# Kernel tuning notes

Measured on AMD Instinct MI355X. Metric: run time of the kernel, lower is better.

## Reference

```python
import jax, jax.numpy as jnp
import numpy as np

# ---- static config (matches init_kwargs) ----
N_BANDS = 8
WIN = 2048
R = 0.5
SR = 16000
STRIDE = WIN - int(R * WIN)  # 1024
Q = 0.707  # torchaudio default Q for high/lowpass_biquad


def _hp_coeffs(cutoff):
    w0 = 2.0 * np.pi * cutoff / SR
    alpha = np.sin(w0) / (2.0 * Q)
    cw = np.cos(w0)
    b0 = (1.0 + cw) / 2.0
    b1 = -(1.0 + cw)
    b2 = (1.0 + cw) / 2.0
    a0 = 1.0 + alpha
    a1 = -2.0 * cw
    a2 = 1.0 - alpha
    return tuple(np.float32(v / a0) for v in (b0, b1, b2, a1, a2))


def _lp_coeffs(cutoff):
    w0 = 2.0 * np.pi * cutoff / SR
    alpha = np.sin(w0) / (2.0 * Q)
    cw = np.cos(w0)
    b0 = (1.0 - cw) / 2.0
    b1 = 1.0 - cw
    b2 = (1.0 - cw) / 2.0
    a0 = 1.0 + alpha
    a1 = -2.0 * cw
    a2 = 1.0 - alpha
    return tuple(np.float32(v / a0) for v in (b0, b1, b2, a1, a2))


# fixed weighting biquad: b=(1,-2,1), a=(1,-1.8,0.81), already a0-normalized
_WEIGHT = (np.float32(1.0), np.float32(-2.0), np.float32(1.0), np.float32(-1.8), np.float32(0.81))


def _biquad(x, coefs):
    """Direct-form I biquad along the last axis; zero initial conditions (matches torchaudio lfilter)."""
    b0, b1, b2, a1, a2 = coefs
    shape = x.shape
    flat = x.reshape(-1, shape[-1])  # [rows, T]
    z = jnp.zeros((flat.shape[0],), dtype=x.dtype)

    def step(carry, xt):
        x1, x2, y1, y2 = carry
        y = b0 * xt + b1 * x1 + b2 * x2 - a1 * y1 - a2 * y2
        return (xt, x1, y, y1), y

    _, ys = jax.lax.scan(step, (z, z, z, z), flat.T)  # ys: [T, rows]
    return jnp.moveaxis(ys, 0, 1).reshape(shape)


def _unfold(x):
    """x: [batch, T] -> [batch, n_seg, WIN] with stride STRIDE (torch.unfold semantics)."""
    T = x.shape[1]
    n_seg = (T - WIN) // STRIDE + 1
    idx = jnp.arange(n_seg)[:, None] * STRIDE + jnp.arange(WIN)[None, :]
    return x[:, idx]


def _loudness(segments):
    weighted = _biquad(segments, _WEIGHT)
    energy = jnp.mean(weighted * weighted, axis=-1)  # [batch, n_seg]
    return 10.0 * jnp.log10(energy + 1e-8)


def _forward(signal, watermark):
    losses = []
    for i in range(N_BANDS):
        low_cut = i * SR / (2 * N_BANDS)
        high_cut = (i + 1) * SR / (2 * N_BANDS)
        hp = _hp_coeffs(low_cut)
        lp = _lp_coeffs(high_cut)
        band_sig = _biquad(_biquad(signal, hp), lp)
        band_wm = _biquad(_biquad(watermark, hp), lp)
        loud_sig = _loudness(_unfold(band_sig))
        loud_wm = _loudness(_unfold(band_wm))
        losses.append(jnp.mean(jnp.abs(loud_wm - loud_sig)))
    return jnp.mean(jnp.stack(losses))


def setup_inputs() -> dict:
    key = jax.random.key(0)
    k1, k2 = jax.random.split(key)
    signal = jax.random.normal(k1, (32, 160000), dtype=jnp.float32)
    watermark = jax.random.normal(k2, (32, 160000), dtype=jnp.float32)
    return {"signal": signal, "watermark": watermark}


def reference(signal, watermark):
    return _forward(signal, watermark)
```

## Files before the change

kernel.cpp:

```cpp
#include <hip/hip_runtime.h>
#include <cmath>

#ifndef M_PI
#define M_PI 3.14159265358979323846
#endif

#define T_LEN   160000
#define NSEG    155
#define ROWS    32
#define NBANDS  8

#define CHUNK   256
#define NSUB    4
#define NQ      16
#define QPC     64
#define NCHUNK  624
#define TOT_IT  (NCHUNK + 2)
#define LOUD_FLOATS (NBANDS * 2 * ROWS * NSEG)

struct AllCoefs {
    float h[NBANDS][5];
    float l[NBANDS][5];
};

__device__ __forceinline__ void barrier_lds_only() {
    asm volatile("s_waitcnt lgkmcnt(0)\n\ts_barrier" ::: "memory");
}

__global__ __launch_bounds__(192, 1)
void tf_pipe3_kernel(const float* __restrict__ sig, const float* __restrict__ wm,
                     float* __restrict__ loud, AllCoefs C) {
    __shared__ float I1[2][CHUNK * 32];
    __shared__ float I2[2][CHUNK * 32];

    const int band = blockIdx.x;
    const int src  = blockIdx.y;
    const int tid  = threadIdx.x;
    const int wid  = tid >> 6;
    const int lane = tid & 63;
    const int ch   = lane & 31;

    const float hb0 = C.h[band][0], hb1 = C.h[band][1], hb2 = C.h[band][2];
    const float hna1 = -C.h[band][3], hna2 = -C.h[band][4];
    const float lb0 = C.l[band][0], lb1 = C.l[band][1], lb2 = C.l[band][2];
    const float lna1 = -C.l[band][3], lna2 = -C.l[band][4];
    const float NA1 =  1.79999995231628417969f;
    const float NA2 = -0.810000002384185791f;

    const float* __restrict__ xrow = (src ? wm : sig) + (size_t)ch * T_LEN;
    const float4* __restrict__ xq  = (const float4*)xrow;

    float x1 = 0.f, x2 = 0.f, y1 = 0.f, y2 = 0.f, acc = 0.f;

    float4 pfA[NQ], pfB[NQ];
    if (wid == 0 && lane < 32) {
        #pragma unroll
        for (int i = 0; i < NQ; ++i) pfA[i] = xq[i];
    }

#define HPF(xx, ff) { float s1_ = __fmaf_rn(hb0, xx, __fmul_rn(hb1, x1)); \
                      ff = __fmaf_rn(hb2, x2, s1_); x2 = x1; x1 = xx; }
#define HPR(ff, oo) { float s3_ = __fmaf_rn(hna1, y1, ff); \
                      oo = __fmaf_rn(hna2, y2, s3_); y2 = y1; y1 = oo; }
#define LPF(xx, ff) { float s1_ = __fmaf_rn(lb0, xx, __fmul_rn(lb1, x1)); \
                      ff = __fmaf_rn(lb2, x2, s1_); x2 = x1; x1 = xx; }
#define LPR(ff, oo) { float s3_ = __fmaf_rn(lna1, y1, ff); \
                      oo = __fmaf_rn(lna2, y2, s3_); y2 = y1; y1 = oo; }
#define WF(xx, ff)  { float s1_ = __fmaf_rn(-2.0f, x1, xx); \
                      ff = __fadd_rn(s1_, x2); x2 = x1; x1 = xx; }
#define WR(ff)      { float s3_ = __fmaf_rn(NA1, y1, ff); \
                      float yy_ = __fmaf_rn(NA2, y2, s3_); \
                      y2 = y1; y1 = yy_; acc = __fmaf_rn(yy_, yy_, acc); }

#define W0SUB(USE, FILL, cc, s, NEXTQ)                                       \
    {                                                                        \
        float4* __restrict__ ob = (float4*)I1[(cc) & 1];                     \
        float4 f[NQ];                                                        \
        _Pragma("unroll")                                                    \
        for (int i = 0; i < NQ; ++i) {                                       \
            float4 v = USE[i];                                               \
            FILL[i] = xq[(NEXTQ) + i];                                       \
            HPF(v.x, f[i].x) HPF(v.y, f[i].y) HPF(v.z, f[i].z) HPF(v.w, f[i].w) \
        }                                                                    \
        _Pragma("unroll")                                                    \
        for (int i = 0; i < NQ; ++i) {                                       \
            float4 o;                                                        \
            HPR(f[i].x, o.x) HPR(f[i].y, o.y) HPR(f[i].z, o.z) HPR(f[i].w, o.w) \
            ob[((s) * NQ + i) * 32 + ch] = o;                                \
        }                                                                    \
    }

    for (int iter = 0; iter < TOT_IT; ++iter) {
        if (wid == 0) {
            if (iter < NCHUNK && lane < 32) {
                const int c = iter;
                const int q0 = c * QPC;
                W0SUB(pfA, pfB, c, 0, q0 + 1 * NQ)
                W0SUB(pfB, pfA, c, 1, q0 + 2 * NQ)
                W0SUB(pfA, pfB, c, 2, q0 + 3 * NQ)
                W0SUB(pfB, pfA, c, 3, q0 + 4 * NQ)
            }
        } else if (wid == 1) {
            if (iter >= 1 && iter <= NCHUNK && lane < 32) {
                const int c = iter - 1;
                const float4* __restrict__ ib = (const float4*)I1[c & 1];
                float4* __restrict__ ob = (float4*)I2[c & 1];
                #pragma unroll
                for (int s = 0; s < NSUB; ++s) {
                    float4 v[NQ];
                    #pragma unroll
                    for (int i = 0; i < NQ; ++i) v[i] = ib[(s * NQ + i) * 32 + ch];
                    float4 f[NQ];
                    #pragma unroll
                    for (int i = 0; i < NQ; ++i) {
                        LPF(v[i].x, f[i].x) LPF(v[i].y, f[i].y)
                        LPF(v[i].z, f[i].z) LPF(v[i].w, f[i].w)
                    }
                    #pragma unroll
                    for (int i = 0; i < NQ; ++i) {
                        float4 o;
                        LPR(f[i].x, o.x) LPR(f[i].y, o.y)
                        LPR(f[i].z, o.z) LPR(f[i].w, o.w)
                        ob[(s * NQ + i) * 32 + ch] = o;
                    }
                }
            }
        } else {
            if (iter >= 2) {
                const int c = iter - 2;
                const bool evenHalf = (lane < 32);
                const float4* __restrict__ ib = (const float4*)I2[c & 1];
                #pragma unroll
                for (int s = 0; s < NSUB; ++s) {
                    const int u = c * NSUB + s;
                    const int m32 = u & 31;
                    const bool rst = (m32 == (evenHalf ? 0 : 16)) && ((u >> 4) < NSEG);
                    if (rst) { x1 = 0.f; x2 = 0.f; }
                    float4 v[NQ];
                    #pragma unroll
                    for (int i = 0; i < NQ; ++i) v[i] = ib[(s * NQ + i) * 32 + ch];
                    float4 f[NQ];
                    #pragma unroll
                    for (int i = 0; i < NQ; ++i) {
                        WF(v[i].x, f[i].x) WF(v[i].y, f[i].y)
                        WF(v[i].z, f[i].z) WF(v[i].w, f[i].w)
                    }
                    if (rst) { y1 = 0.f; y2 = 0.f; acc = 0.f; }
                    #pragma unroll
                    for (int i = 0; i < NQ; ++i) {
                        WR(f[i].x) WR(f[i].y) WR(f[i].z) WR(f[i].w)
                    }
                    const int endm = evenHalf ? 31 : 15;
                    if (m32 == endm && u >= 31) {
                        const int j = (u - 31) >> 4;
                        float e = __fmul_rn(acc, 0.00048828125f);
                        loud[((size_t)((band * 2 + src) * ROWS + ch)) * NSEG + j] =
                            __fmul_rn(10.0f, log10f(__fadd_rn(e, 1e-8f)));
                    }
                }
            }
        }
        barrier_lds_only();
    }
#undef W0SUB
#undef HPF
#undef HPR
#undef LPF
#undef LPR
#undef WF
#undef WR
}

__global__ __launch_bounds__(256)
void tf_reduce_kernel(const float* __restrict__ loud, float* __restrict__ out) {
    __shared__ double sh[256];
    const int per_band = ROWS * NSEG;
    const int npairs   = NBANDS * per_band;
    double s = 0.0;
    for (int idx = threadIdx.x; idx < npairs; idx += 256) {
        int band = idx / per_band;
        int rs   = idx - band * per_band;
        float a = loud[(size_t)(band * 2 + 0) * per_band + rs];
        float b = loud[(size_t)(band * 2 + 1) * per_band + rs];
        s += fabs((double)b - (double)a);
    }
    sh[threadIdx.x] = s;
    __syncthreads();
    for (int off = 128; off > 0; off >>= 1) {
        if (threadIdx.x < off) sh[threadIdx.x] += sh[threadIdx.x + off];
        __syncthreads();
    }
    if (threadIdx.x == 0) out[0] = (float)(sh[0] / (double)npairs);
}

static void mk_hp(double cutoff, float* o) {
    const double w0    = 2.0 * M_PI * cutoff / 16000.0;
    const double alpha = sin(w0) / (2.0 * 0.707);
    const double cw    = cos(w0);
    const double b0 = (1.0 + cw) / 2.0;
    const double b1 = -(1.0 + cw);
    const double b2 = (1.0 + cw) / 2.0;
    const double a0 = 1.0 + alpha;
    const double a1 = -2.0 * cw;
    const double a2 = 1.0 - alpha;
    o[0] = (float)(b0 / a0); o[1] = (float)(b1 / a0); o[2] = (float)(b2 / a0);
    o[3] = (float)(a1 / a0); o[4] = (float)(a2 / a0);
}

static void mk_lp(double cutoff, float* o) {
    const double w0    = 2.0 * M_PI * cutoff / 16000.0;
    const double alpha = sin(w0) / (2.0 * 0.707);
    const double cw    = cos(w0);
    const double b0 = (1.0 - cw) / 2.0;
    const double b1 = 1.0 - cw;
    const double b2 = (1.0 - cw) / 2.0;
    const double a0 = 1.0 + alpha;
    const double a1 = -2.0 * cw;
    const double a2 = 1.0 - alpha;
    o[0] = (float)(b0 / a0); o[1] = (float)(b1 / a0); o[2] = (float)(b2 / a0);
    o[3] = (float)(a1 / a0); o[4] = (float)(a2 / a0);
}

extern "C" void kernel_launch(void* const* d_in, const int* in_sizes, int n_in,
                              void* d_out, int out_size, void* d_ws, size_t ws_size,
                              hipStream_t stream) {
    const float* sig = (const float*)d_in[0];
    const float* wm  = (const float*)d_in[1];
    float* loud = (float*)d_ws;

    AllCoefs C;
    for (int i = 0; i < NBANDS; ++i) {
        mk_hp(1000.0 * (double)i,       C.h[i]);
        mk_lp(1000.0 * (double)(i + 1), C.l[i]);
    }

    tf_pipe3_kernel<<<dim3(NBANDS, 2), 192, 0, stream>>>(sig, wm, loud, C);
    tf_reduce_kernel<<<1, 256, 0, stream>>>(loud, (float*)d_out);
}
```

Baseline: 2.312 ms.

## Split biquad pipeline into six wave stages with FIR/IIR halves separated

The three-wave pipeline (highpass, lowpass, weighting) becomes six waves, with each biquad's feedforward FIR part and recursive IIR part running in separate waves. Chunks shrink to 128 samples and LDS buffers are triple-buffered so each stage runs one chunk behind the previous one. The weighting filter's segment-start reset is handled by saving the first two input samples in a side buffer and patching them into the recursive stage. The aim is to shorten the serial critical path per wave so more of the dependent FMA chains overlap. In exchange there are twice as many barriers, the pipeline is deeper, and the extra LDS round trips add traffic.

```diff
diff --git a/kernel.cpp b/kernel.cpp
--- a/kernel.cpp
+++ b/kernel.cpp
@@ -10,12 +10,10 @@
 #define ROWS    32
 #define NBANDS  8
 
-#define CHUNK   256
-#define NSUB    4
-#define NQ      16
-#define QPC     64
-#define NCHUNK  624
-#define TOT_IT  (NCHUNK + 2)
+#define CHUNK   128
+#define NQC     32
+#define NCHUNK  1248
+#define TOT_IT  (NCHUNK + 5)
 #define LOUD_FLOATS (NBANDS * 2 * ROWS * NSEG)
 
 struct AllCoefs {
@@ -27,11 +25,13 @@
     asm volatile("s_waitcnt lgkmcnt(0)\n\ts_barrier" ::: "memory");
 }
 
-__global__ __launch_bounds__(192, 1)
-void tf_pipe3_kernel(const float* __restrict__ sig, const float* __restrict__ wm,
+__global__ __launch_bounds__(384, 1)
+void tf_pipe6_kernel(const float* __restrict__ sig, const float* __restrict__ wm,
                      float* __restrict__ loud, AllCoefs C) {
-    __shared__ float I1[2][CHUNK * 32];
-    __shared__ float I2[2][CHUNK * 32];
+    __shared__ float4 fA[3][NQC * 32];
+    __shared__ float4 fB[3][NQC * 32];
+    __shared__ float4 fC[2][NQC * 32];
+    __shared__ float  PS[2][2][32];
 
     const int band = blockIdx.x;
     const int src  = blockIdx.y;
@@ -52,123 +52,162 @@
 
     float x1 = 0.f, x2 = 0.f, y1 = 0.f, y2 = 0.f, acc = 0.f;
 
-    float4 pfA[NQ], pfB[NQ];
+    float4 pfA_[16], pfB_[16];
     if (wid == 0 && lane < 32) {
         #pragma unroll
-        for (int i = 0; i < NQ; ++i) pfA[i] = xq[i];
-    }
-
-#define HPF(xx, ff) { float s1_ = __fmaf_rn(hb0, xx, __fmul_rn(hb1, x1)); \
-                      ff = __fmaf_rn(hb2, x2, s1_); x2 = x1; x1 = xx; }
-#define HPR(ff, oo) { float s3_ = __fmaf_rn(hna1, y1, ff); \
-                      oo = __fmaf_rn(hna2, y2, s3_); y2 = y1; y1 = oo; }
-#define LPF(xx, ff) { float s1_ = __fmaf_rn(lb0, xx, __fmul_rn(lb1, x1)); \
-                      ff = __fmaf_rn(lb2, x2, s1_); x2 = x1; x1 = xx; }
-#define LPR(ff, oo) { float s3_ = __fmaf_rn(lna1, y1, ff); \
-                      oo = __fmaf_rn(lna2, y2, s3_); y2 = y1; y1 = oo; }
-#define WF(xx, ff)  { float s1_ = __fmaf_rn(-2.0f, x1, xx); \
-                      ff = __fadd_rn(s1_, x2); x2 = x1; x1 = xx; }
-#define WR(ff)      { float s3_ = __fmaf_rn(NA1, y1, ff); \
-                      float yy_ = __fmaf_rn(NA2, y2, s3_); \
-                      y2 = y1; y1 = yy_; acc = __fmaf_rn(yy_, yy_, acc); }
-
-#define W0SUB(USE, FILL, cc, s, NEXTQ)                                       \
-    {                                                                        \
-        float4* __restrict__ ob = (float4*)I1[(cc) & 1];                     \
-        float4 f[NQ];                                                        \
-        _Pragma("unroll")                                                    \
-        for (int i = 0; i < NQ; ++i) {                                       \
-            float4 v = USE[i];                                               \
-            FILL[i] = xq[(NEXTQ) + i];                                       \
-            HPF(v.x, f[i].x) HPF(v.y, f[i].y) HPF(v.z, f[i].z) HPF(v.w, f[i].w) \
-        }                                                                    \
-        _Pragma("unroll")                                                    \
-        for (int i = 0; i < NQ; ++i) {                                       \
-            float4 o;                                                        \
-            HPR(f[i].x, o.x) HPR(f[i].y, o.y) HPR(f[i].z, o.z) HPR(f[i].w, o.w) \
-            ob[((s) * NQ + i) * 32 + ch] = o;                                \
-        }                                                                    \
-    }
+        for (int i = 0; i < 16; ++i) pfA_[i] = xq[i];
+    }
+
+#define FH(xx, oo) { float s1_ = __fmaf_rn(hb0, xx, __fmul_rn(hb1, x1)); \
+                     oo = __fmaf_rn(hb2, x2, s1_); x2 = x1; x1 = xx; }
+#define RH(ff, oo) { float s3_ = __fmaf_rn(hna1, y1, ff); \
+                     oo = __fmaf_rn(hna2, y2, s3_); y2 = y1; y1 = oo; }
+#define FL(xx, oo) { float s1_ = __fmaf_rn(lb0, xx, __fmul_rn(lb1, x1)); \
+                     oo = __fmaf_rn(lb2, x2, s1_); x2 = x1; x1 = xx; }
+#define RL(ff, oo) { float s3_ = __fmaf_rn(lna1, y1, ff); \
+                     oo = __fmaf_rn(lna2, y2, s3_); y2 = y1; y1 = oo; }
+#define FW(xx, oo) { float s1_ = __fmaf_rn(-2.0f, x1, xx); \
+                     oo = __fadd_rn(s1_, x2); x2 = x1; x1 = xx; }
+#define RW(ff)     { float s3_ = __fmaf_rn(NA1, y1, ff); \
+                     float yy_ = __fmaf_rn(NA2, y2, s3_); \
+                     y2 = y1; y1 = yy_; acc = __fmaf_rn(yy_, yy_, acc); }
 
     for (int iter = 0; iter < TOT_IT; ++iter) {
         if (wid == 0) {
-            if (iter < NCHUNK && lane < 32) {
-                const int c = iter;
-                const int q0 = c * QPC;
-                W0SUB(pfA, pfB, c, 0, q0 + 1 * NQ)
-                W0SUB(pfB, pfA, c, 1, q0 + 2 * NQ)
-                W0SUB(pfA, pfB, c, 2, q0 + 3 * NQ)
-                W0SUB(pfB, pfA, c, 3, q0 + 4 * NQ)
+            const int c = iter;
+            if (c < NCHUNK && lane < 32) {
+                float4* __restrict__ ob = fA[c % 3];
+                #pragma unroll
+                for (int i = 0; i < 16; ++i) {
+                    float4 v = pfA_[i];
+                    pfB_[i] = xq[(2 * c + 1) * 16 + i];
+                    float4 o;
+                    FH(v.x, o.x) FH(v.y, o.y) FH(v.z, o.z) FH(v.w, o.w)
+                    ob[i * 32 + ch] = o;
+                }
+                #pragma unroll
+                for (int i = 0; i < 16; ++i) {
+                    float4 v = pfB_[i];
+                    pfA_[i] = xq[(2 * c + 2) * 16 + i];
+                    float4 o;
+                    FH(v.x, o.x) FH(v.y, o.y) FH(v.z, o.z) FH(v.w, o.w)
+                    ob[(16 + i) * 32 + ch] = o;
+                }
+            }
+        } else if (wid == 4) {
+            const int c = iter - 1;
+            if (c >= 0 && c < NCHUNK && lane < 32) {
+                float4* __restrict__ b = fA[c % 3];
+                #pragma unroll
+                for (int g = 0; g < 2; ++g) {
+                    float4 v[16];
+                    #pragma unroll
+                    for (int i = 0; i < 16; ++i) v[i] = b[(g * 16 + i) * 32 + ch];
+                    #pragma unroll
+                    for (int i = 0; i < 16; ++i) {
+                        float4 o;
+                        RH(v[i].x, o.x) RH(v[i].y, o.y) RH(v[i].z, o.z) RH(v[i].w, o.w)
+                        b[(g * 16 + i) * 32 + ch] = o;
+                    }
+                }
             }
         } else if (wid == 1) {
-            if (iter >= 1 && iter <= NCHUNK && lane < 32) {
-                const int c = iter - 1;
-                const float4* __restrict__ ib = (const float4*)I1[c & 1];
-                float4* __restrict__ ob = (float4*)I2[c & 1];
-                #pragma unroll
-                for (int s = 0; s < NSUB; ++s) {
-                    float4 v[NQ];
-                    #pragma unroll
-                    for (int i = 0; i < NQ; ++i) v[i] = ib[(s * NQ + i) * 32 + ch];
-                    float4 f[NQ];
-                    #pragma unroll
-                    for (int i = 0; i < NQ; ++i) {
-                        LPF(v[i].x, f[i].x) LPF(v[i].y, f[i].y)
-                        LPF(v[i].z, f[i].z) LPF(v[i].w, f[i].w)
-                    }
-                    #pragma unroll
-                    for (int i = 0; i < NQ; ++i) {
-                        float4 o;
-                        LPR(f[i].x, o.x) LPR(f[i].y, o.y)
-                        LPR(f[i].z, o.z) LPR(f[i].w, o.w)
-                        ob[(s * NQ + i) * 32 + ch] = o;
+            const int c = iter - 2;
+            if (c >= 0 && c < NCHUNK && lane < 32) {
+                const float4* __restrict__ ib = fA[c % 3];
+                float4* __restrict__ ob = fB[c % 3];
+                #pragma unroll
+                for (int g = 0; g < 2; ++g) {
+                    float4 v[16];
+                    #pragma unroll
+                    for (int i = 0; i < 16; ++i) v[i] = ib[(g * 16 + i) * 32 + ch];
+                    #pragma unroll
+                    for (int i = 0; i < 16; ++i) {
+                        float4 o;
+                        FL(v[i].x, o.x) FL(v[i].y, o.y) FL(v[i].z, o.z) FL(v[i].w, o.w)
+                        ob[(g * 16 + i) * 32 + ch] = o;
+                    }
+                }
+            }
+        } else if (wid == 5) {
+            const int c = iter - 3;
+            if (c >= 0 && c < NCHUNK && lane < 32) {
+                float4* __restrict__ b = fB[c % 3];
+                #pragma unroll
+                for (int g = 0; g < 2; ++g) {
+                    float4 v[16];
+                    #pragma unroll
+                    for (int i = 0; i < 16; ++i) v[i] = b[(g * 16 + i) * 32 + ch];
+                    #pragma unroll
+                    for (int i = 0; i < 16; ++i) {
+                        float4 o;
+                        RL(v[i].x, o.x) RL(v[i].y, o.y) RL(v[i].z, o.z) RL(v[i].w, o.w)
+                        b[(g * 16 + i) * 32 + ch] = o;
+                    }
+                }
+            }
+        } else if (wid == 2) {
+            const int c = iter - 4;
+            if (c >= 0 && c < NCHUNK && lane < 32) {
+                const float4* __restrict__ ib = fB[c % 3];
+                float4* __restrict__ ob = fC[c & 1];
+                #pragma unroll
+                for (int g = 0; g < 2; ++g) {
+                    float4 v[16];
+                    #pragma unroll
+                    for (int i = 0; i < 16; ++i) v[i] = ib[(g * 16 + i) * 32 + ch];
+                    if (g == 0 && (c & 7) == 0) {
+                        PS[c & 1][0][ch] = v[0].x;
+                        PS[c & 1][1][ch] = v[0].y;
+                    }
+                    #pragma unroll
+                    for (int i = 0; i < 16; ++i) {
+                        float4 o;
+                        FW(v[i].x, o.x) FW(v[i].y, o.y) FW(v[i].z, o.z) FW(v[i].w, o.w)
+                        ob[(g * 16 + i) * 32 + ch] = o;
                     }
                 }
             }
         } else {
-            if (iter >= 2) {
-                const int c = iter - 2;
-                const bool evenHalf = (lane < 32);
-                const float4* __restrict__ ib = (const float4*)I2[c & 1];
-                #pragma unroll
-                for (int s = 0; s < NSUB; ++s) {
-                    const int u = c * NSUB + s;
-                    const int m32 = u & 31;
-                    const bool rst = (m32 == (evenHalf ? 0 : 16)) && ((u >> 4) < NSEG);
-                    if (rst) { x1 = 0.f; x2 = 0.f; }
-                    float4 v[NQ];
-                    #pragma unroll
-                    for (int i = 0; i < NQ; ++i) v[i] = ib[(s * NQ + i) * 32 + ch];
-                    float4 f[NQ];
-                    #pragma unroll
-                    for (int i = 0; i < NQ; ++i) {
-                        WF(v[i].x, f[i].x) WF(v[i].y, f[i].y)
-                        WF(v[i].z, f[i].z) WF(v[i].w, f[i].w)
-                    }
-                    if (rst) { y1 = 0.f; y2 = 0.f; acc = 0.f; }
-                    #pragma unroll
-                    for (int i = 0; i < NQ; ++i) {
-                        WR(f[i].x) WR(f[i].y) WR(f[i].z) WR(f[i].w)
-                    }
-                    const int endm = evenHalf ? 31 : 15;
-                    if (m32 == endm && u >= 31) {
-                        const int j = (u - 31) >> 4;
-                        float e = __fmul_rn(acc, 0.00048828125f);
-                        loud[((size_t)((band * 2 + src) * ROWS + ch)) * NSEG + j] =
-                            __fmul_rn(10.0f, log10f(__fadd_rn(e, 1e-8f)));
-                    }
+            const int c = iter - 5;
+            if (c >= 0 && c < NCHUNK) {
+                const bool EVh = (lane < 32);
+                const float4* __restrict__ ib = fC[c & 1];
+                const float ps0 = PS[c & 1][0][ch];
+                const float ps1 = PS[c & 1][1][ch];
+                const bool rst = ((c & 15) == (EVh ? 0 : 8)) && ((c >> 3) < NSEG);
+                if (rst) { y1 = 0.f; y2 = 0.f; acc = 0.f; }
+                #pragma unroll
+                for (int g = 0; g < 2; ++g) {
+                    float4 v[16];
+                    #pragma unroll
+                    for (int i = 0; i < 16; ++i) v[i] = ib[(g * 16 + i) * 32 + ch];
+                    if (g == 0 && rst) {
+                        v[0].x = ps0;
+                        v[0].y = __fmaf_rn(-2.0f, ps0, ps1);
+                    }
+                    #pragma unroll
+                    for (int i = 0; i < 16; ++i) {
+                        RW(v[i].x) RW(v[i].y) RW(v[i].z) RW(v[i].w)
+                    }
+                }
+                const bool endf = ((c & 15) == (EVh ? 15 : 7)) && (c >= 15);
+                if (endf) {
+                    const int j = (c - 15) >> 3;
+                    float e = __fmul_rn(acc, 0.00048828125f);
+                    loud[((size_t)((band * 2 + src) * ROWS + ch)) * NSEG + j] =
+                        __fmul_rn(10.0f, log10f(__fadd_rn(e, 1e-8f)));
                 }
             }
         }
         barrier_lds_only();
     }
-#undef W0SUB
-#undef HPF
-#undef HPR
-#undef LPF
-#undef LPR
-#undef WF
-#undef WR
+#undef FH
+#undef RH
+#undef FL
+#undef RL
+#undef FW
+#undef RW
 }
 
 __global__ __launch_bounds__(256)
@@ -234,6 +273,6 @@
         mk_lp(1000.0 * (double)(i + 1), C.l[i]);
     }
 
-    tf_pipe3_kernel<<<dim3(NBANDS, 2), 192, 0, stream>>>(sig, wm, loud, C);
+    tf_pipe6_kernel<<<dim3(NBANDS, 2), 384, 0, stream>>>(sig, wm, loud, C);
     tf_reduce_kernel<<<1, 256, 0, stream>>>(loud, (float*)d_out);
 }
```

New measurement: 2.152 ms. 1.07x faster.
